# Performance work log

Hardware: AMD Instinct MI355X
Metric: run time of the kernel (lower is better)

The kernel has to match this reference:

```python
import jax, jax.numpy as jnp
import numpy as np

B, T, D, H = 256, 256, 512, 8
HD = D // H  # 64


def _rope_tables(t, hd):
    pos = jnp.arange(t, dtype=jnp.float32)
    inv_freq = 1.0 / (10000.0 ** (jnp.arange(0, hd, 2, dtype=jnp.float32) / hd))
    ang = pos[:, None] * inv_freq[None, :]            # (T, hd/2)
    cos = jnp.repeat(jnp.cos(ang), 2, axis=-1)        # (T, hd) interleaved pairs
    sin = jnp.repeat(jnp.sin(ang), 2, axis=-1)
    return cos, sin


def setup_inputs() -> dict:
    key = jax.random.key(0)
    k1, k2, k3 = jax.random.split(key, 3)
    x = jax.random.normal(k1, (B, T, D), dtype=jnp.float32)
    cos, sin = _rope_tables(T, HD)
    Wqkv = jax.random.normal(k2, (3 * D, D), dtype=jnp.float32) * 0.02
    Wout = jax.random.normal(k3, (D, D), dtype=jnp.float32) * 0.02
    return {"x": x, "cos": cos, "sin": sin, "Wqkv": Wqkv, "Wout": Wout}


def _apply_rope(x, cos, sin):
    # x: (B, T, H, hd); cos/sin: (T, hd)
    x1 = x[..., 0::2]
    x2 = x[..., 1::2]
    rot = jnp.stack((-x2, x1), axis=-1).reshape(x.shape)  # interleaved rotate
    return x * cos[None, :, None, :] + rot * sin[None, :, None, :]


def reference(x, cos, sin, Wqkv, Wout):
    b, t, d = x.shape
    qkv = (x @ Wqkv.T).reshape(b, t, 3, H, HD)
    q, k, v = qkv[:, :, 0], qkv[:, :, 1], qkv[:, :, 2]   # (B, T, H, hd)
    q = _apply_rope(q, cos[:t], sin[:t])
    k = _apply_rope(k, cos[:t], sin[:t])
    q = q.transpose(0, 2, 1, 3)  # (B, H, T, hd)
    k = k.transpose(0, 2, 1, 3)
    v = v.transpose(0, 2, 1, 3)
    scale = 1.0 / jnp.sqrt(jnp.float32(HD))
    scores = jnp.einsum('bhqd,bhkd->bhqk', q, k) * scale
    causal = jnp.arange(t)[:, None] >= jnp.arange(t)[None, :]  # (T, T)
    scores = jnp.where(causal[None, None], scores, jnp.finfo(scores.dtype).min)
    att = jax.nn.softmax(scores, axis=-1)
    out = jnp.einsum('bhqk,bhkd->bhqd', att, v)          # (B, H, T, hd)
    out = out.transpose(0, 2, 1, 3).reshape(b, t, d)
    return out @ Wout.T
```

## Files before the change

### kernel.cpp

```cpp
#include <hip/hip_runtime.h>

typedef float floatx4 __attribute__((ext_vector_type(4)));
typedef short short8 __attribute__((ext_vector_type(8)));
typedef unsigned short ushort_t;

#define AS1 __attribute__((address_space(1)))
#define AS3 __attribute__((address_space(3)))

__device__ __forceinline__ void gload_lds16(const ushort_t* g, ushort_t* l) {
    __builtin_amdgcn_global_load_lds((const AS1 unsigned int*)g, (AS3 unsigned int*)l, 16, 0, 0);
}

__device__ __forceinline__ ushort_t f2bf(float f) {
    union { float f; unsigned u; } v; v.f = f;
    unsigned r = v.u + 0x7FFFu + ((v.u >> 16) & 1u);
    return (ushort_t)(r >> 16);
}

#define KDIM 512
#define LOG2E 1.44269504f

#define XB_OFF   0ull
#define ATT_OFF  0ull
#define WQKV_OFF 33554432ull
#define WOUT_OFF 34340864ull
#define QB_OFF   34603008ull
#define KB_OFF   68157440ull
#define VB_OFF   101711872ull

__global__ __launch_bounds__(256) void convert_k(
    const float* __restrict__ x, const float* __restrict__ wqkv,
    const float* __restrict__ wout, ushort_t* __restrict__ dst)
{
    size_t i = (size_t)blockIdx.x * 256 + threadIdx.x;
    size_t e = i * 4;
    const float* s; size_t o;
    if (e < 33554432ull)      { s = x;    o = e; }
    else if (e < 34340864ull) { s = wqkv; o = e - 33554432ull; }
    else                      { s = wout; o = e - 34340864ull; }
    float4 v = *(const float4*)(s + o);
    ushort4 r;
    r.x = f2bf(v.x); r.y = f2bf(v.y); r.z = f2bf(v.z); r.w = f2bf(v.w);
    *(ushort4*)(dst + e) = r;
}

template <int EPI>
__global__ __launch_bounds__(256, 3) void gemm_bt(
    const ushort_t* __restrict__ A, const ushort_t* __restrict__ Bw,
    float* __restrict__ Cf,
    ushort_t* __restrict__ qout, ushort_t* __restrict__ kout, ushort_t* __restrict__ vout,
    const float* __restrict__ cosT, const float* __restrict__ sinT)
{
    __shared__ __align__(16) ushort_t As[128 * 64];
    __shared__ __align__(16) ushort_t Bs[128 * 64];
    const int bn = blockIdx.x, bm = blockIdx.y;
    const int tid = threadIdx.x;
    const int lane = tid & 63, wave = tid >> 6;
    const int wm = wave & 1, wn = wave >> 1;
    const int quad = lane >> 4, l16 = lane & 15;

    const ushort_t* Ag = A + (size_t)bm * 128 * KDIM;
    const ushort_t* Bg = Bw + (size_t)bn * 128 * KDIM;

    floatx4 acc[4][4] = {};

    for (int k0 = 0; k0 < KDIM; k0 += 64) {
#pragma unroll
        for (int ii = 0; ii < 4; ii++) {
            int e8 = ii * 256 + tid;
            int row = e8 >> 3, col = (e8 & 7) << 3;
            gload_lds16(Ag + row * KDIM + k0 + col, &As[e8 * 8]);
            gload_lds16(Bg + row * KDIM + k0 + col, &Bs[e8 * 8]);
        }
        __syncthreads();
#pragma unroll
        for (int kk = 0; kk < 2; kk++) {
            short8 af[4], bf[4];
#pragma unroll
            for (int mi = 0; mi < 4; mi++)
                af[mi] = *(const short8*)&As[(wm * 64 + mi * 16 + l16) * 64 + kk * 32 + quad * 8];
#pragma unroll
            for (int ni = 0; ni < 4; ni++)
                bf[ni] = *(const short8*)&Bs[(wn * 64 + ni * 16 + l16) * 64 + kk * 32 + quad * 8];
#pragma unroll
            for (int mi = 0; mi < 4; mi++)
#pragma unroll
                for (int ni = 0; ni < 4; ni++)
                    acc[mi][ni] = __builtin_amdgcn_mfma_f32_16x16x32_bf16(
                        af[mi], bf[ni], acc[mi][ni], 0, 0, 0);
        }
        __syncthreads();
    }

    if constexpr (EPI == 1) {
        const int n_base = bn * 128 + wn * 64;
        const int qkv = n_base >> 9;
        ushort_t* dst = (qkv == 0) ? qout : (qkv == 1 ? kout : vout);
#pragma unroll
        for (int mi = 0; mi < 4; mi++) {
            const int m = bm * 128 + wm * 64 + mi * 16 + quad * 4;
#pragma unroll
            for (int ni = 0; ni < 4; ni++) {
                const int n = n_base + ni * 16 + l16;
                const int nw = n & 511, hd = n & 63;
#pragma unroll
                for (int r = 0; r < 4; r++) {
                    const int mm = m + r, t = mm & 255;
                    const size_t dsti = (size_t)mm * 512 + nw;
                    float val = acc[mi][ni][r];
                    if (qkv == 2) {
                        dst[dsti] = f2bf(val);
                    } else {
                        float partner = __shfl_xor(val, 1);
                        float c = cosT[t * 64 + hd], s = sinT[t * 64 + hd];
                        float o = val * c + ((hd & 1) ? partner : -partner) * s;
                        dst[dsti] = (qkv == 0) ? f2bf(o * 0.125f) : f2bf(o);
                    }
                }
            }
        }
    } else {
#pragma unroll
        for (int mi = 0; mi < 4; mi++) {
            const int m = bm * 128 + wm * 64 + mi * 16 + quad * 4;
#pragma unroll
            for (int ni = 0; ni < 4; ni++) {
                const int n = bn * 128 + wn * 64 + ni * 16 + l16;
#pragma unroll
                for (int r = 0; r < 4; r++)
                    Cf[(size_t)(m + r) * 512 + n] = acc[mi][ni][r];
            }
        }
    }
}

__global__ __launch_bounds__(256) void attn_k(
    const ushort_t* __restrict__ qb, const ushort_t* __restrict__ kb,
    const ushort_t* __restrict__ vb, ushort_t* __restrict__ attb)
{
    __shared__ __align__(16) ushort_t Ks[256 * 72];
    __shared__ __align__(16) ushort_t Vt[64 * 264];
    __shared__ __align__(16) ushort_t Ps[4 * 32 * 40];

    const int blk = blockIdx.x;
    const int qt = blk & 1, bh = blk >> 1;
    const int b = bh >> 3, h = bh & 7;
    const int tid = threadIdx.x, lane = tid & 63, w = tid >> 6;
    const int quad = lane >> 4, l16 = lane & 15;
    const int q0 = qt * 128;
    const int kend = q0 + 128;

    const ushort_t* Kg = kb + ((size_t)b * 256) * 512 + h * 64;
    const ushort_t* Vg = vb + ((size_t)b * 256) * 512 + h * 64;
    const ushort_t* Qg = qb + ((size_t)b * 256) * 512 + h * 64;

    for (int e8 = tid; e8 < kend * 8; e8 += 256) {
        int t = e8 >> 3, c = (e8 & 7) << 3;
        *(short8*)&Ks[t * 72 + c] = *(const short8*)&Kg[t * 512 + c];
        short8 vv = *(const short8*)&Vg[t * 512 + c];
#pragma unroll
        for (int j = 0; j < 8; j++) Vt[(c + j) * 264 + t] = ((const ushort_t*)&vv)[j];
    }
    __syncthreads();

    short8 qf[2][2];
#pragma unroll
    for (int mi = 0; mi < 2; mi++)
#pragma unroll
        for (int kk = 0; kk < 2; kk++)
            qf[mi][kk] = *(const short8*)&Qg[(size_t)(q0 + w * 32 + mi * 16 + l16) * 512 + kk * 32 + quad * 8];

    float lsum[2][4] = {};
    floatx4 o_[2][4] = {};

    ushort_t* Pw = &Ps[w * 32 * 40];
    const int ktdiag = qt * 4 + w;

    for (int kt = 0; kt <= ktdiag; kt++) {
        const bool diag = (kt == ktdiag);
        floatx4 s_[2][2] = {};
#pragma unroll
        for (int kk = 0; kk < 2; kk++) {
            short8 kf0 = *(const short8*)&Ks[(kt * 32 + l16) * 72 + kk * 32 + quad * 8];
            short8 kf1 = *(const short8*)&Ks[(kt * 32 + 16 + l16) * 72 + kk * 32 + quad * 8];
#pragma unroll
            for (int mi = 0; mi < 2; mi++) {
                s_[mi][0] = __builtin_amdgcn_mfma_f32_16x16x32_bf16(qf[mi][kk], kf0, s_[mi][0], 0, 0, 0);
                s_[mi][1] = __builtin_amdgcn_mfma_f32_16x16x32_bf16(qf[mi][kk], kf1, s_[mi][1], 0, 0, 0);
            }
        }
#pragma unroll
        for (int mi = 0; mi < 2; mi++) {
#pragma unroll
            for (int r = 0; r < 4; r++) {
                float p0 = exp2f(s_[mi][0][r] * LOG2E);
                float p1 = exp2f(s_[mi][1][r] * LOG2E);
                if (diag) {
                    const int rl = mi * 16 + quad * 4 + r;
                    if (l16 > rl)      p0 = 0.f;
                    if (l16 + 16 > rl) p1 = 0.f;
                }
                lsum[mi][r] += p0 + p1;
                const int rowL = mi * 16 + quad * 4 + r;
                Pw[rowL * 40 + l16] = f2bf(p0);
                Pw[rowL * 40 + 16 + l16] = f2bf(p1);
            }
        }
        __asm__ volatile("s_waitcnt lgkmcnt(0)" ::: "memory");
        short8 pf[2];
#pragma unroll
        for (int mi = 0; mi < 2; mi++)
            pf[mi] = *(const short8*)&Pw[(mi * 16 + l16) * 40 + quad * 8];
#pragma unroll
        for (int vni = 0; vni < 4; vni++) {
            short8 vf = *(const short8*)&Vt[(vni * 16 + l16) * 264 + kt * 32 + quad * 8];
#pragma unroll
            for (int mi = 0; mi < 2; mi++)
                o_[mi][vni] = __builtin_amdgcn_mfma_f32_16x16x32_bf16(pf[mi], vf, o_[mi][vni], 0, 0, 0);
        }
    }

#pragma unroll
    for (int mi = 0; mi < 2; mi++) {
#pragma unroll
        for (int r = 0; r < 4; r++) {
            float rs = lsum[mi][r];
            rs += __shfl_xor(rs, 1);
            rs += __shfl_xor(rs, 2);
            rs += __shfl_xor(rs, 4);
            rs += __shfl_xor(rs, 8);
            const float inv = 1.f / rs;
            const int t = q0 + w * 32 + mi * 16 + quad * 4 + r;
            const size_t base = ((size_t)(b * 256 + t)) * 512 + h * 64;
#pragma unroll
            for (int vni = 0; vni < 4; vni++)
                attb[base + vni * 16 + l16] = f2bf(o_[mi][vni][r] * inv);
        }
    }
}

extern "C" void kernel_launch(void* const* d_in, const int* in_sizes, int n_in,
                              void* d_out, int out_size, void* d_ws, size_t ws_size,
                              hipStream_t stream) {
    const float* x    = (const float*)d_in[0];
    const float* cosT = (const float*)d_in[1];
    const float* sinT = (const float*)d_in[2];
    const float* wqkv = (const float*)d_in[3];
    const float* wout = (const float*)d_in[4];
    float* out = (float*)d_out;
    ushort_t* ws = (ushort_t*)d_ws;

    ushort_t* xb    = ws + XB_OFF;
    ushort_t* wqkvb = ws + WQKV_OFF;
    ushort_t* woutb = ws + WOUT_OFF;
    ushort_t* qbp   = ws + QB_OFF;
    ushort_t* kbp   = ws + KB_OFF;
    ushort_t* vbp   = ws + VB_OFF;
    ushort_t* attb  = ws + ATT_OFF;

    convert_k<<<33792, 256, 0, stream>>>(x, wqkv, wout, ws);
    gemm_bt<1><<<dim3(12, 512), 256, 0, stream>>>(xb, wqkvb, nullptr, qbp, kbp, vbp, cosT, sinT);
    attn_k<<<4096, 256, 0, stream>>>(qbp, kbp, vbp, attb);
    gemm_bt<0><<<dim3(4, 512), 256, 0, stream>>>(attb, woutb, out, nullptr, nullptr, nullptr, nullptr, nullptr);
}
```

Measured before the change: 584.8 us.

## Swizzle LDS layouts, stage epilogue stores through LDS, remap blocks across XCDs

The GEMM tiles are split into two 32-wide k-halves so each LDS row is 64 bytes, which changes the bank pattern of the MFMA operand reads. The QKV GEMM epilogue now writes rotated bf16 results into swizzled LDS and then emits 16-byte coalesced global stores, replacing scattered 2-byte stores. Attention gets an XOR-swizzled transposed V layout to cut bank conflicts and an LDS-staged output store. Block indices are remapped round-robin across the 8 XCDs for locality, and the fp32 output store loop is reordered. The extra LDS round trips and syncs add some latency in exchange.

```diff
diff --git a/kernel.cpp b/kernel.cpp
--- a/kernel.cpp
+++ b/kernel.cpp
@@ -19,6 +19,7 @@
 
 #define KDIM 512
 #define LOG2E 1.44269504f
+#define LGKM0 do { asm volatile("s_waitcnt lgkmcnt(0)" ::: "memory"); __builtin_amdgcn_sched_barrier(0); } while (0)
 
 #define XB_OFF   0ull
 #define ATT_OFF  0ull
@@ -51,9 +52,12 @@
     ushort_t* __restrict__ qout, ushort_t* __restrict__ kout, ushort_t* __restrict__ vout,
     const float* __restrict__ cosT, const float* __restrict__ sinT)
 {
-    __shared__ __align__(16) ushort_t As[128 * 64];
-    __shared__ __align__(16) ushort_t Bs[128 * 64];
-    const int bn = blockIdx.x, bm = blockIdx.y;
+    __shared__ __align__(16) ushort_t As[2 * 128 * 32];
+    __shared__ __align__(16) ushort_t Bs[2 * 128 * 32];
+    constexpr int NBN = (EPI == 1) ? 12 : 4;
+    const int f = blockIdx.x;
+    const int wkr = (f & 7) * (NBN * 64) + (f >> 3);
+    const int bm = wkr / NBN, bn = wkr % NBN;
     const int tid = threadIdx.x;
     const int lane = tid & 63, wave = tid >> 6;
     const int wm = wave & 1, wn = wave >> 1;
@@ -66,22 +70,23 @@
 
     for (int k0 = 0; k0 < KDIM; k0 += 64) {
 #pragma unroll
-        for (int ii = 0; ii < 4; ii++) {
-            int e8 = ii * 256 + tid;
-            int row = e8 >> 3, col = (e8 & 7) << 3;
-            gload_lds16(Ag + row * KDIM + k0 + col, &As[e8 * 8]);
-            gload_lds16(Bg + row * KDIM + k0 + col, &Bs[e8 * 8]);
+        for (int it = 0; it < 4; it++) {
+            const int e = it * 256 + tid;
+            const int kh = e >> 9, rem = e & 511;
+            const int row = rem >> 2, c8 = (rem & 3) << 3;
+            gload_lds16(Ag + row * KDIM + k0 + kh * 32 + c8, &As[e * 8]);
+            gload_lds16(Bg + row * KDIM + k0 + kh * 32 + c8, &Bs[e * 8]);
         }
         __syncthreads();
 #pragma unroll
-        for (int kk = 0; kk < 2; kk++) {
+        for (int kh = 0; kh < 2; kh++) {
             short8 af[4], bf[4];
 #pragma unroll
             for (int mi = 0; mi < 4; mi++)
-                af[mi] = *(const short8*)&As[(wm * 64 + mi * 16 + l16) * 64 + kk * 32 + quad * 8];
+                af[mi] = *(const short8*)&As[kh * 4096 + (wm * 64 + mi * 16 + l16) * 32 + quad * 8];
 #pragma unroll
             for (int ni = 0; ni < 4; ni++)
-                bf[ni] = *(const short8*)&Bs[(wn * 64 + ni * 16 + l16) * 64 + kk * 32 + quad * 8];
+                bf[ni] = *(const short8*)&Bs[kh * 4096 + (wn * 64 + ni * 16 + l16) * 32 + quad * 8];
 #pragma unroll
             for (int mi = 0; mi < 4; mi++)
 #pragma unroll
@@ -96,42 +101,62 @@
         const int n_base = bn * 128 + wn * 64;
         const int qkv = n_base >> 9;
         ushort_t* dst = (qkv == 0) ? qout : (qkv == 1 ? kout : vout);
+        ushort_t* Ep = (wave < 2) ? (As + wave * 4096) : (Bs + (wave - 2) * 4096);
+        const int nb = n_base & 511;
 #pragma unroll
         for (int mi = 0; mi < 4; mi++) {
-            const int m = bm * 128 + wm * 64 + mi * 16 + quad * 4;
 #pragma unroll
             for (int ni = 0; ni < 4; ni++) {
-                const int n = n_base + ni * 16 + l16;
-                const int nw = n & 511, hd = n & 63;
 #pragma unroll
                 for (int r = 0; r < 4; r++) {
-                    const int mm = m + r, t = mm & 255;
-                    const size_t dsti = (size_t)mm * 512 + nw;
+                    const int row = mi * 16 + quad * 4 + r;
+                    const int m = bm * 128 + wm * 64 + row;
+                    const int tt = m & 255;
+                    const int col = ni * 16 + l16;
+                    const int hd = col;
                     float val = acc[mi][ni][r];
+                    float o;
                     if (qkv == 2) {
-                        dst[dsti] = f2bf(val);
+                        o = val;
                     } else {
                         float partner = __shfl_xor(val, 1);
-                        float c = cosT[t * 64 + hd], s = sinT[t * 64 + hd];
-                        float o = val * c + ((hd & 1) ? partner : -partner) * s;
-                        dst[dsti] = (qkv == 0) ? f2bf(o * 0.125f) : f2bf(o);
+                        float c = cosT[tt * 64 + hd], s = sinT[tt * 64 + hd];
+                        o = val * c + ((hd & 1) ? partner : -partner) * s;
+                        if (qkv == 0) o *= 0.125f;
                     }
+                    const int colp = col ^ (quad << 4);
+                    Ep[row * 64 + colp] = f2bf(o);
                 }
             }
         }
+        LGKM0;
+#pragma unroll
+        for (int t8 = 0; t8 < 8; t8++) {
+            const int row = t8 * 8 + (lane >> 3);
+            const int c0 = (lane & 7) * 8;
+            const int colp = c0 ^ (((row >> 2) & 3) << 4);
+            short8 v = *(const short8*)&Ep[row * 64 + colp];
+            const int m = bm * 128 + wm * 64 + row;
+            *(short8*)&dst[(size_t)m * 512 + nb + c0] = v;
+        }
     } else {
 #pragma unroll
         for (int mi = 0; mi < 4; mi++) {
-            const int m = bm * 128 + wm * 64 + mi * 16 + quad * 4;
-#pragma unroll
-            for (int ni = 0; ni < 4; ni++) {
-                const int n = bn * 128 + wn * 64 + ni * 16 + l16;
-#pragma unroll
-                for (int r = 0; r < 4; r++)
-                    Cf[(size_t)(m + r) * 512 + n] = acc[mi][ni][r];
-            }
-        }
-    }
+#pragma unroll
+            for (int r = 0; r < 4; r++) {
+                const int m = bm * 128 + wm * 64 + mi * 16 + quad * 4 + r;
+#pragma unroll
+                for (int ni = 0; ni < 4; ni++) {
+                    const int n = bn * 128 + wn * 64 + ni * 16 + l16;
+                    Cf[(size_t)m * 512 + n] = acc[mi][ni][r];
+                }
+            }
+        }
+    }
+}
+
+__device__ __forceinline__ int vt_addr(int d, int t) {
+    return d * 264 + (t & 7) + ((((t >> 3) ^ (d >> 3)) & 31) << 3);
 }
 
 __global__ __launch_bounds__(256) void attn_k(
@@ -142,8 +167,9 @@
     __shared__ __align__(16) ushort_t Vt[64 * 264];
     __shared__ __align__(16) ushort_t Ps[4 * 32 * 40];
 
-    const int blk = blockIdx.x;
-    const int qt = blk & 1, bh = blk >> 1;
+    const int f = blockIdx.x;
+    const int wkr = (f & 7) * 512 + (f >> 3);
+    const int qt = wkr & 1, bh = wkr >> 1;
     const int b = bh >> 3, h = bh & 7;
     const int tid = threadIdx.x, lane = tid & 63, w = tid >> 6;
     const int quad = lane >> 4, l16 = lane & 15;
@@ -159,7 +185,7 @@
         *(short8*)&Ks[t * 72 + c] = *(const short8*)&Kg[t * 512 + c];
         short8 vv = *(const short8*)&Vg[t * 512 + c];
 #pragma unroll
-        for (int j = 0; j < 8; j++) Vt[(c + j) * 264 + t] = ((const ushort_t*)&vv)[j];
+        for (int j = 0; j < 8; j++) Vt[vt_addr(c + j, t)] = ((const ushort_t*)&vv)[j];
     }
     __syncthreads();
 
@@ -213,13 +239,15 @@
             pf[mi] = *(const short8*)&Pw[(mi * 16 + l16) * 40 + quad * 8];
 #pragma unroll
         for (int vni = 0; vni < 4; vni++) {
-            short8 vf = *(const short8*)&Vt[(vni * 16 + l16) * 264 + kt * 32 + quad * 8];
+            short8 vf = *(const short8*)&Vt[vt_addr(vni * 16 + l16, kt * 32 + quad * 8)];
 #pragma unroll
             for (int mi = 0; mi < 2; mi++)
                 o_[mi][vni] = __builtin_amdgcn_mfma_f32_16x16x32_bf16(pf[mi], vf, o_[mi][vni], 0, 0, 0);
         }
     }
 
+    __syncthreads();
+    ushort_t* Ow = Ks + w * 2304;
 #pragma unroll
     for (int mi = 0; mi < 2; mi++) {
 #pragma unroll
@@ -230,12 +258,24 @@
             rs += __shfl_xor(rs, 4);
             rs += __shfl_xor(rs, 8);
             const float inv = 1.f / rs;
-            const int t = q0 + w * 32 + mi * 16 + quad * 4 + r;
-            const size_t base = ((size_t)(b * 256 + t)) * 512 + h * 64;
-#pragma unroll
-            for (int vni = 0; vni < 4; vni++)
-                attb[base + vni * 16 + l16] = f2bf(o_[mi][vni][r] * inv);
-        }
+            const int rowL = mi * 16 + quad * 4 + r;
+#pragma unroll
+            for (int vni = 0; vni < 4; vni++) {
+                const int col = vni * 16 + l16;
+                const int g = (col >> 3) ^ (rowL >> 3);
+                Ow[rowL * 72 + (col & 7) + (g << 3)] = f2bf(o_[mi][vni][r] * inv);
+            }
+        }
+    }
+    LGKM0;
+#pragma unroll
+    for (int it = 0; it < 4; it++) {
+        const int rowL = it * 8 + (lane >> 3);
+        const int c0 = (lane & 7) * 8;
+        const int g = (lane & 7) ^ it;
+        short8 v = *(const short8*)&Ow[rowL * 72 + (g << 3)];
+        const int t = q0 + w * 32 + rowL;
+        *(short8*)&attb[((size_t)(b * 256 + t)) * 512 + h * 64 + c0] = v;
     }
 }
 
@@ -259,7 +299,7 @@
     ushort_t* attb  = ws + ATT_OFF;
 
     convert_k<<<33792, 256, 0, stream>>>(x, wqkv, wout, ws);
-    gemm_bt<1><<<dim3(12, 512), 256, 0, stream>>>(xb, wqkvb, nullptr, qbp, kbp, vbp, cosT, sinT);
+    gemm_bt<1><<<6144, 256, 0, stream>>>(xb, wqkvb, nullptr, qbp, kbp, vbp, cosT, sinT);
     attn_k<<<4096, 256, 0, stream>>>(qbp, kbp, vbp, attb);
-    gemm_bt<0><<<dim3(4, 512), 256, 0, stream>>>(attb, woutb, out, nullptr, nullptr, nullptr, nullptr, nullptr);
-}
+    gemm_bt<0><<<2048, 256, 0, stream>>>(attb, woutb, out, nullptr, nullptr, nullptr, nullptr, nullptr);
+}
```

Measured after the change: 543.4 us. -7.1%, faster.
